# Kernel optimization log

Measured on AMD Instinct MI355X. Metric: run time of the kernel, lower is better.

## Reference

```python
import jax, jax.numpy as jnp
import numpy as np

D_MODEL = 1024
D_STATE = 16
D_CONV = 4
EXPAND = 2
D_INNER = EXPAND * D_MODEL  # 2048
DT_RANK = 64  # ceil(1024/16)
BATCH = 2
SEQ = 1024
EPS = 1e-5


def _causal_depthwise_conv(x, w, b):
    # x: (B, L, D); w: (D, K) depthwise kernel; b: (D,)
    K = w.shape[1]
    xp = jnp.pad(x, ((0, 0), (K - 1, 0), (0, 0)))            # left-pad for causality
    out = jax.lax.conv_general_dilated(
        xp.transpose(0, 2, 1),          # (B, D, L+K-1)
        w[:, None, :],                  # (D, 1, K)
        window_strides=(1,), padding='VALID',
        feature_group_count=w.shape[0])
    return out.transpose(0, 2, 1) + b   # (B, L, D)


def _ssm_dir(xs, conv_w, conv_b, xproj_w, dt_w, dt_b, A_log, D_skip):
    # xs: (B, L, D_INNER)
    Bsz = xs.shape[0]
    xc = jax.nn.silu(_causal_depthwise_conv(xs, conv_w, conv_b))
    x_dbl = xc @ xproj_w                                        # (B, L, dt_rank + 2N)
    dt, B_ssm, C_ssm = jnp.split(x_dbl, [DT_RANK, DT_RANK + D_STATE], axis=-1)
    dt = jax.nn.softplus(dt @ dt_w + dt_b)                      # (B, L, D_INNER)
    A = -jnp.exp(A_log)                                         # (D_INNER, N)
    dA = jnp.exp(dt[..., None] * A)                             # (B, L, D_INNER, N)
    dBu = dt[..., None] * B_ssm[:, :, None, :] * xc[..., None]  # (B, L, D_INNER, N)

    def step(h, inp):
        dAt, dBut, ct = inp          # (B,D,N), (B,D,N), (B,N)
        h = dAt * h + dBut
        y = jnp.einsum('bdn,bn->bd', h, ct)
        return h, y

    h0 = jnp.zeros((Bsz, D_INNER, D_STATE), dtype=xs.dtype)
    _, ys = jax.lax.scan(step, h0,
                         (jnp.moveaxis(dA, 1, 0), jnp.moveaxis(dBu, 1, 0), jnp.moveaxis(C_ssm, 1, 0)))
    y = jnp.moveaxis(ys, 0, 1)                                  # (B, L, D_INNER)
    return y + xc * D_skip


def _layernorm(x, gamma, beta):
    mu = jnp.mean(x, axis=-1, keepdims=True)
    var = jnp.mean(jnp.square(x - mu), axis=-1, keepdims=True)
    return (x - mu) * jax.lax.rsqrt(var + EPS) * gamma + beta


def setup_inputs() -> dict:
    key = jax.random.key(0)
    ks = jax.random.split(key, 24)
    s = 0.02
    A_init = jnp.log(jnp.tile(jnp.arange(1, D_STATE + 1, dtype=jnp.float32)[None, :], (D_INNER, 1)))
    # dt bias init (inverse-softplus of small dt), as in the torch module
    dt0 = jnp.exp(jax.random.uniform(ks[20], (D_INNER,)) * (np.log(0.1) - np.log(0.001)) + np.log(0.001))
    dt0 = jnp.clip(dt0, 1e-4)
    inv_dt = dt0 + jnp.log(-jnp.expm1(-dt0))
    return {
        'x': jax.random.normal(ks[0], (BATCH, SEQ, D_MODEL), jnp.float32),
        'gamma': jnp.ones((D_MODEL,), jnp.float32),
        'beta': jnp.zeros((D_MODEL,), jnp.float32),
        'in_w': jax.random.normal(ks[1], (D_MODEL, 2 * D_INNER), jnp.float32) * s,
        'conv_w': jax.random.normal(ks[2], (D_INNER, D_CONV), jnp.float32) * s,
        'conv_b': jnp.zeros((D_INNER,), jnp.float32),
        'xproj_w': jax.random.normal(ks[3], (D_INNER, DT_RANK + 2 * D_STATE), jnp.float32) * s,
        'dt_w': jax.random.normal(ks[4], (DT_RANK, D_INNER), jnp.float32) * s,
        'dt_b': inv_dt,
        'A_log': A_init,
        'D_skip': jnp.ones((D_INNER,), jnp.float32),
        'conv_w_b': jax.random.normal(ks[5], (D_INNER, D_CONV), jnp.float32) * s,
        'conv_b_b': jnp.zeros((D_INNER,), jnp.float32),
        'xproj_w_b': jax.random.normal(ks[6], (D_INNER, DT_RANK + 2 * D_STATE), jnp.float32) * s,
        'dt_w_b': jax.random.normal(ks[7], (DT_RANK, D_INNER), jnp.float32) * s,
        'dt_b_b': inv_dt,
        'A_log_b': A_init,
        'D_skip_b': jnp.ones((D_INNER,), jnp.float32),
        'merge_w': jax.random.normal(ks[8], (2 * D_INNER, D_INNER), jnp.float32) * s,
        'out_w': jax.random.normal(ks[9], (D_INNER, D_MODEL), jnp.float32) * s,
    }


def reference(x, gamma, beta, in_w, conv_w, conv_b, xproj_w, dt_w, dt_b, A_log, D_skip,
              conv_w_b, conv_b_b, xproj_w_b, dt_w_b, dt_b_b, A_log_b, D_skip_b,
              merge_w, out_w):
    residual = x
    h = _layernorm(x, gamma, beta)
    xz = h @ in_w                               # (B, L, 2*D_INNER)
    xs, z = jnp.split(xz, 2, axis=-1)
    y_fwd = _ssm_dir(xs, conv_w, conv_b, xproj_w, dt_w, dt_b, A_log, D_skip)
    y_back = _ssm_dir(xs[:, ::-1], conv_w_b, conv_b_b, xproj_w_b, dt_w_b, dt_b_b, A_log_b, D_skip_b)[:, ::-1]
    y = jnp.concatenate([y_fwd, y_back], axis=-1) @ merge_w
    y = y * jax.nn.silu(z)
    y = y @ out_w
    return residual + y
```

## Files before the change

### kernel.cpp

```cpp
#include <hip/hip_runtime.h>
#include <hip/hip_bf16.h>
#include <math.h>

typedef __hip_bfloat16 bf16;
typedef unsigned int u32;
typedef __attribute__((ext_vector_type(8))) short bf16x8;
typedef __attribute__((ext_vector_type(4))) float f32x4;

#define BATCH 2
#define SEQ 1024
#define DM 1024
#define DI 2048
#define NST 16
#define DTR 64
#define XDN 96
#define XDP_LD 128
#define T_TOK 2048
#define N2 4096
#define NCHUNK 32
#define CLEN 32

static __device__ __forceinline__ float b2f(bf16 v) { return __bfloat162float(v); }
static __device__ __forceinline__ float bits2f(unsigned short u) {
    return __uint_as_float(((unsigned)u) << 16);
}

static __device__ __forceinline__ float softplus_fast(float t) {
    return (t > 20.f) ? t : __logf(1.f + __expf(t));
}

static __device__ __forceinline__ void gload_lds16(const void* g, void* l) {
    __builtin_amdgcn_global_load_lds((__attribute__((address_space(1))) u32*)(size_t)g,
                                     (__attribute__((address_space(3))) u32*)l, 16, 0, 0);
}

#define SBAR() do { asm volatile("" ::: "memory"); __builtin_amdgcn_s_barrier(); asm volatile("" ::: "memory"); } while (0)

static __device__ void tileT(const float* __restrict__ in, bf16* __restrict__ out,
                             int K, int N, int t, float (*tb)[33]) {
    int nt = N >> 5;
    int bx = (t % nt) << 5, by = (t / nt) << 5;
    int tx = threadIdx.x & 31, r0 = threadIdx.x >> 5;
#pragma unroll
    for (int r = r0; r < 32; r += 8)
        tb[r][tx] = in[(size_t)(by + r) * N + bx + tx];
    __syncthreads();
#pragma unroll
    for (int r = r0; r < 32; r += 8)
        out[(size_t)(bx + r) * K + by + tx] = __float2bfloat16(tb[tx][r]);
}

#define LN_BLKS   T_TOK
#define INW_T     ((N2 / 32) * (DM / 32))
#define OUTW_T    ((DM / 32) * (DI / 32))
#define MRGW_T    ((DI / 32) * (N2 / 32))
#define SMALL_BLK ((2 * XDP_LD * DI + 2 * DI * DTR) / 256)

__global__ __launch_bounds__(256) void prep_mega(const float* __restrict__ x,
                                                 const float* __restrict__ gamma,
                                                 const float* __restrict__ beta,
                                                 bf16* __restrict__ H,
                                                 const float* __restrict__ in_w, bf16* __restrict__ in_wT,
                                                 const float* __restrict__ out_w, bf16* __restrict__ out_wT,
                                                 const float* __restrict__ merge_w, bf16* __restrict__ merge_wT,
                                                 const float* __restrict__ xpf, const float* __restrict__ xpb,
                                                 bf16* __restrict__ XPF, bf16* __restrict__ XPB,
                                                 const float* __restrict__ dtwf, const float* __restrict__ dtwb,
                                                 bf16* __restrict__ dtwT) {
    __shared__ float tbuf[32][33];
    __shared__ float red[8];
    int bid = blockIdx.x;
    int tid = threadIdx.x;

    if (bid < LN_BLKS) {
        int t = bid;
        float xv[4];
        float s = 0.f, s2 = 0.f;
#pragma unroll
        for (int k = 0; k < 4; ++k) {
            float v = x[(size_t)t * DM + k * 256 + tid];
            xv[k] = v; s += v; s2 += v * v;
        }
#pragma unroll
        for (int off = 32; off; off >>= 1) {
            s  += __shfl_down(s, off);
            s2 += __shfl_down(s2, off);
        }
        int wid = tid >> 6, lane = tid & 63;
        if (!lane) { red[wid] = s; red[4 + wid] = s2; }
        __syncthreads();
        if (tid == 0) {
            float S = red[0] + red[1] + red[2] + red[3];
            float S2 = red[4] + red[5] + red[6] + red[7];
            float mu = S * (1.f / DM);
            float var = S2 * (1.f / DM) - mu * mu;
            red[0] = mu;
            red[1] = rsqrtf(var + 1e-5f);
        }
        __syncthreads();
        float mu = red[0], rs = red[1];
#pragma unroll
        for (int k = 0; k < 4; ++k) {
            int i = k * 256 + tid;
            H[(size_t)t * DM + i] = __float2bfloat16((xv[k] - mu) * rs * gamma[i] + beta[i]);
        }
        return;
    }
    bid -= LN_BLKS;
    if (bid < INW_T)  { tileT(in_w, in_wT, DM, N2, bid, tbuf); return; }
    bid -= INW_T;
    if (bid < OUTW_T) { tileT(out_w, out_wT, DI, DM, bid, tbuf); return; }
    bid -= OUTW_T;
    if (bid < MRGW_T) { tileT(merge_w, merge_wT, N2, DI, bid, tbuf); return; }
    bid -= MRGW_T;
    int idx = bid * 256 + tid;
    if (idx < 2 * XDP_LD * DI) {
        int dir = idx >= XDP_LD * DI;
        int i = idx - dir * (XDP_LD * DI);
        int n = i >> 11;
        int k = i & (DI - 1);
        float v = (n < XDN) ? (dir ? xpb : xpf)[k * XDN + n] : 0.f;
        (dir ? XPB : XPF)[i] = __float2bfloat16(v);
    } else {
        int j = idx - 2 * XDP_LD * DI;
        int dir = j >= DI * DTR;
        int e = j - dir * (DI * DTR);
        int n = e >> 6;
        int k = e & 63;
        dtwT[(size_t)dir * DI * DTR + n * DTR + k] =
            __float2bfloat16((dir ? dtwb : dtwf)[(size_t)k * DI + n]);
    }
}

template <int EPI>
__global__ __launch_bounds__(256) void mfma_gemm(const bf16* __restrict__ A,
                                                 const bf16* __restrict__ BT,
                                                 const bf16* __restrict__ BT2, int bysplit,
                                                 bf16* __restrict__ Cb,
                                                 const float* __restrict__ resid,
                                                 float* __restrict__ outf,
                                                 bf16* __restrict__ Pb,
                                                 const float* __restrict__ bias1,
                                                 const float* __restrict__ bias2,
                                                 int M, int N, int K) {
    __shared__ bf16 As[8192];
    __shared__ bf16 Bs[8192];
    int tid = threadIdx.x;
    int wave = tid >> 6, lane = tid & 63;
    int q = lane >> 4, ln16 = lane & 15;
    int bm = blockIdx.y * 128, bn = blockIdx.x * 128;
    int wm = (wave >> 1) * 64, wn = (wave & 1) * 64;
    const bf16* Bt = ((int)blockIdx.y < bysplit) ? BT : BT2;

    int ks = K / gridDim.z;
    int kb = blockIdx.z * ks;

    f32x4 zf; zf[0] = zf[1] = zf[2] = zf[3] = 0.f;
    f32x4 acc[4][4];
#pragma unroll
    for (int i = 0; i < 4; ++i)
#pragma unroll
        for (int j = 0; j < 4; ++j) acc[i][j] = zf;

    for (int k0 = kb; k0 < kb + ks; k0 += 64) {
#pragma unroll
        for (int i = 0; i < 4; ++i) {
            int s = wave * 256 + i * 64 + lane;
            int kg = s >> 7, m = s & 127;
            gload_lds16(&A[(size_t)(bm + m) * K + k0 + kg * 8], &As[(wave * 256 + i * 64) * 8]);
            gload_lds16(&Bt[(size_t)(bn + m) * K + k0 + kg * 8], &Bs[(wave * 256 + i * 64) * 8]);
        }
        __syncthreads();
#pragma unroll
        for (int kk = 0; kk < 2; ++kk) {
            bf16x8 af[4], bfr[4];
#pragma unroll
            for (int i = 0; i < 4; ++i) {
                af[i]  = *(const bf16x8*)&As[(((kk * 4 + q) * 128) + (wm + i * 16 + ln16)) * 8];
                bfr[i] = *(const bf16x8*)&Bs[(((kk * 4 + q) * 128) + (wn + i * 16 + ln16)) * 8];
            }
#pragma unroll
            for (int i = 0; i < 4; ++i)
#pragma unroll
                for (int j = 0; j < 4; ++j)
                    acc[i][j] = __builtin_amdgcn_mfma_f32_16x16x32_bf16(af[i], bfr[j], acc[i][j], 0, 0, 0);
        }
        __syncthreads();
    }

    size_t pbase = (size_t)blockIdx.z * M * N;
#pragma unroll
    for (int i = 0; i < 4; ++i)
#pragma unroll
        for (int r = 0; r < 4; ++r) {
            int row = bm + wm + i * 16 + q * 4 + r;
            const float* bias = (EPI == 4) ? ((row < T_TOK) ? bias1 : bias2) : nullptr;
#pragma unroll
            for (int j = 0; j < 4; ++j) {
                int col = bn + wn + j * 16 + ln16;
                size_t idx = (size_t)row * N + col;
                float v = acc[i][j][r];
                if (EPI == 0)      Cb[idx] = __float2bfloat16(v);
                else if (EPI == 1) outf[idx] = resid[idx] + v;
                else if (EPI == 2) outf[idx] = v;
                else if (EPI == 3) Pb[pbase + idx] = __float2bfloat16(v);
                else {
                    Cb[idx] = __float2bfloat16(softplus_fast(v + bias[col]));
                }
            }
        }
}

template <int EPI>
__global__ __launch_bounds__(512, 2) void gemm256(const bf16* __restrict__ A,
                                                  const bf16* __restrict__ BT,
                                                  bf16* __restrict__ Cb,
                                                  bf16* __restrict__ Pb,
                                                  int M, int N, int K) {
    __shared__ bf16 LA[4][8192];
    __shared__ bf16 LB[4][8192];
    int tid = threadIdx.x;
    int wave = tid >> 6, lane = tid & 63;
    int q = lane >> 4, ln16 = lane & 15;

    int gx = gridDim.x, gy = gridDim.y, gz = gridDim.z;
    int L = blockIdx.x + gx * (blockIdx.y + gy * blockIdx.z);
    int nwg = gx * gy * gz;
    int qd = nwg >> 3, rd = nwg & 7;
    int xcd = L & 7, base = L >> 3;
    int wg = (xcd < rd ? xcd * (qd + 1) : rd * (qd + 1) + (xcd - rd) * qd) + base;
    int bxi = wg % gx, byi = (wg / gx) % gy, bzi = wg / (gx * gy);

    int bm = byi * 256, bn = bxi * 256;
    int wm = (wave >> 2) * 128, wn = (wave & 3) * 64;
    int ksz = K / gz;
    int kb = bzi * ksz;
    int NT = ksz >> 5;

    int o0 = tid * 16, o1 = 8192 + tid * 16;
    int r0 = o0 >> 6, r1 = o1 >> 6;
    int c0 = (o0 & 63) ^ (((r0 >> 1) & 3) << 4);
    int c1 = (o1 & 63) ^ (((r1 >> 1) & 3) << 4);
    const bf16* pa0 = &A[(size_t)(bm + r0) * K + kb + (c0 >> 1)];
    const bf16* pa1 = &A[(size_t)(bm + r1) * K + kb + (c1 >> 1)];
    const bf16* pb0 = &BT[(size_t)(bn + r0) * K + kb + (c0 >> 1)];
    const bf16* pb1 = &BT[(size_t)(bn + r1) * K + kb + (c1 >> 1)];
    int d0 = wave * 512;
    int d1 = 4096 + wave * 512;

    int aoff[8], boff[4];
#pragma unroll
    for (int i = 0; i < 8; ++i) {
        int r = wm + i * 16 + ln16;
        aoff[i] = (r * 64 + q * 16) ^ (((r >> 1) & 3) << 4);
    }
#pragma unroll
    for (int j = 0; j < 4; ++j) {
        int r = wn + j * 16 + ln16;
        boff[j] = (r * 64 + q * 16) ^ (((r >> 1) & 3) << 4);
    }

    f32x4 zf; zf[0] = zf[1] = zf[2] = zf[3] = 0.f;
    f32x4 acc[8][4];
#pragma unroll
    for (int i = 0; i < 8; ++i)
#pragma unroll
        for (int j = 0; j < 4; ++j) acc[i][j] = zf;

    auto STAGE = [&](int b, int koff) {
        gload_lds16(pa0 + koff, &LA[b][d0]);
        gload_lds16(pa1 + koff, &LA[b][d1]);
        gload_lds16(pb0 + koff, &LB[b][d0]);
        gload_lds16(pb1 + koff, &LB[b][d1]);
    };

#define RD_FRAGS(AV, BV, TT) do {                                             \
        const bf16* LAb_ = LA[(TT) & 3];                                      \
        const bf16* LBb_ = LB[(TT) & 3];                                      \
        _Pragma("unroll")                                                     \
        for (int j_ = 0; j_ < 4; ++j_) BV[j_] = *(const bf16x8*)&LBb_[boff[j_] >> 1]; \
        _Pragma("unroll")                                                     \
        for (int i_ = 0; i_ < 8; ++i_) AV[i_] = *(const bf16x8*)&LAb_[aoff[i_] >> 1]; \
    } while (0)

#define MFMA_ALL(AV, BV) do {                                                 \
        __builtin_amdgcn_s_setprio(1);                                        \
        _Pragma("unroll")                                                     \
        for (int i_ = 0; i_ < 8; ++i_)                                        \
            _Pragma("unroll")                                                 \
            for (int j_ = 0; j_ < 4; ++j_)                                    \
                acc[i_][j_] = __builtin_amdgcn_mfma_f32_16x16x32_bf16(AV[i_], BV[j_], acc[i_][j_], 0, 0, 0); \
        __builtin_amdgcn_s_setprio(0);                                        \
    } while (0)

    bf16x8 avX[8], bvX[4], avY[8], bvY[4];

    STAGE(0, 0); STAGE(1, 32); STAGE(2, 64);
    asm volatile("s_waitcnt vmcnt(4)" ::: "memory");
    SBAR();
    RD_FRAGS(avX, bvX, 0);

    for (int t = 0; t < NT; t += 2) {
        if (t + 1 < NT) RD_FRAGS(avY, bvY, t + 1);
        if (t + 3 < NT) STAGE((t + 3) & 3, (t + 3) * 32);
        MFMA_ALL(avX, bvX);
        if (t + 3 < NT)      asm volatile("s_waitcnt vmcnt(4)" ::: "memory");
        else if (t + 2 < NT) asm volatile("s_waitcnt vmcnt(0)" ::: "memory");
        SBAR();
        if (t + 2 < NT) RD_FRAGS(avX, bvX, t + 2);
        if (t + 4 < NT) STAGE((t + 4) & 3, (t + 4) * 32);
        MFMA_ALL(avY, bvY);
        if (t + 4 < NT)      asm volatile("s_waitcnt vmcnt(4)" ::: "memory");
        else if (t + 3 < NT) asm volatile("s_waitcnt vmcnt(0)" ::: "memory");
        SBAR();
    }
#undef RD_FRAGS
#undef MFMA_ALL

    size_t pbase = (size_t)bzi * ((size_t)M * N);
#pragma unroll
    for (int i = 0; i < 8; ++i)
#pragma unroll
        for (int r = 0; r < 4; ++r) {
            int row = bm + wm + i * 16 + q * 4 + r;
#pragma unroll
            for (int j = 0; j < 4; ++j) {
                int col = bn + wn + j * 16 + ln16;
                size_t idx = (size_t)row * N + col;
                float v = acc[i][j][r];
                if (EPI == 0) Cb[idx] = __float2bfloat16(v);
                else          Pb[pbase + idx] = __float2bfloat16(v);
            }
        }
}

__global__ __launch_bounds__(256) void reduce_plain(const bf16* __restrict__ P, int ns, size_t MN,
                                                    bf16* __restrict__ O) {
    size_t i = ((size_t)blockIdx.x * 256 + threadIdx.x) * 4;
    float s[4] = {0.f, 0.f, 0.f, 0.f};
    for (int k = 0; k < ns; ++k) {
        ushort4 p = *reinterpret_cast<const ushort4*>(&P[(size_t)k * MN + i]);
        s[0] += bits2f(p.x); s[1] += bits2f(p.y); s[2] += bits2f(p.z); s[3] += bits2f(p.w);
    }
    bf16 r[4];
#pragma unroll
    for (int j = 0; j < 4; ++j) r[j] = __float2bfloat16(s[j]);
    *reinterpret_cast<ushort4*>(&O[i]) = *reinterpret_cast<ushort4*>(r);
}

__global__ __launch_bounds__(256) void reduce_gate(const bf16* __restrict__ P, int ns, size_t MN,
                                                   const bf16* __restrict__ XZ, bf16* __restrict__ YM) {
    size_t i = ((size_t)blockIdx.x * 256 + threadIdx.x) * 4;
    float s[4] = {0.f, 0.f, 0.f, 0.f};
    for (int k = 0; k < ns; ++k) {
        ushort4 p = *reinterpret_cast<const ushort4*>(&P[(size_t)k * MN + i]);
        s[0] += bits2f(p.x); s[1] += bits2f(p.y); s[2] += bits2f(p.z); s[3] += bits2f(p.w);
    }
    int t = (int)(i >> 11), c = (int)(i & (DI - 1));
    const bf16* zp = &XZ[(size_t)t * N2 + DI + c];
    bf16 r[4];
#pragma unroll
    for (int j = 0; j < 4; ++j) {
        float z = b2f(zp[j]);
        r[j] = __float2bfloat16(s[j] * (z / (1.f + __expf(-z))));
    }
    *reinterpret_cast<ushort4*>(&YM[i]) = *reinterpret_cast<ushort4*>(r);
}

__global__ __launch_bounds__(256) void reduce_out(const bf16* __restrict__ P, int ns, size_t MN,
                                                  const float* __restrict__ x, float* __restrict__ out) {
    size_t i = ((size_t)blockIdx.x * 256 + threadIdx.x) * 4;
    float s[4] = {0.f, 0.f, 0.f, 0.f};
    for (int k = 0; k < ns; ++k) {
        ushort4 p = *reinterpret_cast<const ushort4*>(&P[(size_t)k * MN + i]);
        s[0] += bits2f(p.x); s[1] += bits2f(p.y); s[2] += bits2f(p.z); s[3] += bits2f(p.w);
    }
    float4 xv = *reinterpret_cast<const float4*>(&x[i]);
    float4 o = {s[0] + xv.x, s[1] + xv.y, s[2] + xv.z, s[3] + xv.w};
    *reinterpret_cast<float4*>(&out[i]) = o;
}

__global__ __launch_bounds__(256) void reduce_xdbl(const bf16* __restrict__ P, int ns, size_t MN,
                                                   float* __restrict__ XDP, bf16* __restrict__ XDdt) {
    size_t i = ((size_t)blockIdx.x * 256 + threadIdx.x) * 4;
    float s[4] = {0.f, 0.f, 0.f, 0.f};
    for (int k = 0; k < ns; ++k) {
        ushort4 p = *reinterpret_cast<const ushort4*>(&P[(size_t)k * MN + i]);
        s[0] += bits2f(p.x); s[1] += bits2f(p.y); s[2] += bits2f(p.z); s[3] += bits2f(p.w);
    }
    float4 o = {s[0], s[1], s[2], s[3]};
    *reinterpret_cast<float4*>(&XDP[i]) = o;
    int col = (int)(i & (XDP_LD - 1));
    if (col < DTR) {
        size_t row = i >> 7;
        bf16 r[4];
#pragma unroll
        for (int j = 0; j < 4; ++j) r[j] = __float2bfloat16(s[j]);
        *reinterpret_cast<ushort4*>(&XDdt[row * DTR + col]) = *reinterpret_cast<ushort4*>(r);
    }
}

__global__ __launch_bounds__(256) void gemm_dt(const float* __restrict__ A,
                                               const float* __restrict__ Bw,
                                               const float* __restrict__ bias,
                                               bf16* __restrict__ Cb, int M, int N) {
    __shared__ float As[16][68];
    __shared__ float Bs[16][68];
    int tid = threadIdx.x;
    int bm = blockIdx.y * 64, bn = blockIdx.x * 64;
    int tx = tid & 15, ty = tid >> 4;
    float acc[4][4];
#pragma unroll
    for (int i = 0; i < 4; ++i)
#pragma unroll
        for (int j = 0; j < 4; ++j) acc[i][j] = 0.f;
    int arow = tid >> 2, acg = (tid & 3) * 4;
    int brow = tid >> 4, bcol = (tid & 15) * 4;
    for (int k0 = 0; k0 < DTR; k0 += 16) {
        float4 av = *reinterpret_cast<const float4*>(&A[(size_t)(bm + arow) * XDP_LD + k0 + acg]);
        As[acg + 0][arow] = av.x; As[acg + 1][arow] = av.y;
        As[acg + 2][arow] = av.z; As[acg + 3][arow] = av.w;
        float4 bv = *reinterpret_cast<const float4*>(&Bw[(size_t)(k0 + brow) * N + bn + bcol]);
        Bs[brow][bcol + 0] = bv.x; Bs[brow][bcol + 1] = bv.y;
        Bs[brow][bcol + 2] = bv.z; Bs[brow][bcol + 3] = bv.w;
        __syncthreads();
#pragma unroll
        for (int kk = 0; kk < 16; ++kk) {
            float4 a = *reinterpret_cast<const float4*>(&As[kk][ty * 4]);
            float4 b = *reinterpret_cast<const float4*>(&Bs[kk][tx * 4]);
            acc[0][0] += a.x * b.x; acc[0][1] += a.x * b.y; acc[0][2] += a.x * b.z; acc[0][3] += a.x * b.w;
            acc[1][0] += a.y * b.x; acc[1][1] += a.y * b.y; acc[1][2] += a.y * b.z; acc[1][3] += a.y * b.w;
            acc[2][0] += a.z * b.x; acc[2][1] += a.z * b.y; acc[2][2] += a.z * b.z; acc[2][3] += a.z * b.w;
            acc[3][0] += a.w * b.x; acc[3][1] += a.w * b.y; acc[3][2] += a.w * b.z; acc[3][3] += a.w * b.w;
        }
        __syncthreads();
    }
    int row0 = bm + ty * 4, col0 = bn + tx * 4;
#pragma unroll
    for (int i = 0; i < 4; ++i)
#pragma unroll
        for (int j = 0; j < 4; ++j) {
            float v = acc[i][j] + bias[col0 + j];
            Cb[(size_t)(row0 + i) * N + col0 + j] = __float2bfloat16(softplus_fast(v));
        }
}

__global__ __launch_bounds__(256) void conv_kernel(const bf16* __restrict__ XZ,
                                                   const float* __restrict__ wf, const float* __restrict__ bf_,
                                                   const float* __restrict__ wb, const float* __restrict__ bb_,
                                                   bf16* __restrict__ XCF, bf16* __restrict__ XCB) {
    int idx = blockIdx.x * 256 + threadIdx.x;
    int cg = idx & (DI / 8 - 1);
    int c0 = cg * 8;
    int g = idx >> 8;
    int l = g & (SEQ - 1);
    int b = g >> 10;
    float sf[8], sb[8];
    float4 wfv[8], wbv[8];
#pragma unroll
    for (int u = 0; u < 8; ++u) {
        wfv[u] = *(const float4*)&wf[(c0 + u) * 4];
        wbv[u] = *(const float4*)&wb[(c0 + u) * 4];
        sf[u] = bf_[c0 + u];
        sb[u] = bb_[c0 + u];
    }
#pragma unroll
    for (int j = 0; j < 4; ++j) {
        int lf = l - 3 + j;
        if (lf >= 0) {
            bf16x8 v = *(const bf16x8*)&XZ[((size_t)(b * SEQ + lf)) * N2 + c0];
#pragma unroll
            for (int u = 0; u < 8; ++u) {
                float w = (j == 0) ? wfv[u].x : (j == 1) ? wfv[u].y : (j == 2) ? wfv[u].z : wfv[u].w;
                sf[u] += w * bits2f((unsigned short)v[u]);
            }
        }
        int lb = l + 3 - j;
        if (lb < SEQ) {
            bf16x8 v = *(const bf16x8*)&XZ[((size_t)(b * SEQ + lb)) * N2 + c0];
#pragma unroll
            for (int u = 0; u < 8; ++u) {
                float w = (j == 0) ? wbv[u].x : (j == 1) ? wbv[u].y : (j == 2) ? wbv[u].z : wbv[u].w;
                sb[u] += w * bits2f((unsigned short)v[u]);
            }
        }
    }
    bf16 rf[8], rb[8];
#pragma unroll
    for (int u = 0; u < 8; ++u) {
        rf[u] = __float2bfloat16(sf[u] / (1.f + __expf(-sf[u])));
        rb[u] = __float2bfloat16(sb[u] / (1.f + __expf(-sb[u])));
    }
    size_t o = (size_t)g * DI + c0;
    *(bf16x8*)&XCF[o] = *(bf16x8*)rf;
    *(bf16x8*)&XCB[o] = *(bf16x8*)rb;
}

template <int NC, bool FINAL>
__global__ __launch_bounds__(256) void scan_chunk(const bf16* __restrict__ DTF_, const bf16* __restrict__ DTB_,
                                                  const bf16* __restrict__ XCF_, const bf16* __restrict__ XCB_,
                                                  const float* __restrict__ XDP,
                                                  const float* __restrict__ Af, const float* __restrict__ Ab,
                                                  const float* __restrict__ Df, const float* __restrict__ Db,
                                                  float* __restrict__ HLOC, float* __restrict__ SUMDT,
                                                  bf16* __restrict__ YCAT) {
    constexpr int CL = SEQ / NC;
    __shared__ float bsl[CL][32];
    __shared__ bf16 dtl[CL][128];
    __shared__ bf16 xcl[CL][128];
    int tid = threadIdx.x;
    int sg = tid & 1;
    int cl = tid >> 1;
    int cbase = blockIdx.x * 128;
    int c = cbase + cl;
    int b = blockIdx.y;
    int dir = (int)blockIdx.z >= NC;
    int chunk = blockIdx.z - dir * NC;
    const bf16* DT = dir ? DTB_ : DTF_;
    const bf16* XC = dir ? XCB_ : XCF_;
    for (int i = tid; i < CL * 8; i += 256) {
        int it = i >> 3, j4 = (i & 7) * 4;
        int sit = chunk * CL + it;
        int l = dir ? (SEQ - 1 - sit) : sit;
        size_t row = (size_t)dir * T_TOK + (size_t)b * SEQ + l;
        *(float4*)&bsl[it][j4] = *(const float4*)&XDP[row * XDP_LD + DTR + j4];
    }
    for (int ch = tid; ch < CL * 16; ch += 256) {
        int it = ch >> 4, of = (ch & 15) * 8;
        int sit = chunk * CL + it;
        int l = dir ? (SEQ - 1 - sit) : sit;
        size_t g = (size_t)b * SEQ + l;
        *(bf16x8*)&dtl[it][of] = *(const bf16x8*)&DT[g * DI + cbase + of];
        *(bf16x8*)&xcl[it][of] = *(const bf16x8*)&XC[g * DI + cbase + of];
    }
    const float* Al = dir ? Ab : Af;
    int sg8 = sg * 8;
    float A[8];
#pragma unroll
    for (int n = 0; n < 8; ++n) A[n] = -__expf(Al[c * NST + sg8 + n]);
    float aunit = A[0] / (float)(sg8 + 1);
    bool fastp = true;
#pragma unroll
    for (int n = 1; n < 8; ++n) {
        float k = A[n] / aunit;
        fastp = fastp && (fabsf(k - (float)(sg8 + 1 + n)) < 1e-3f);
    }
    size_t base = ((((size_t)dir * BATCH + b) * NC + chunk) * DI + c);
    float h[8];
    float Dv = 0.f;
    if (FINAL) {
#pragma unroll
        for (int n = 0; n < 8; ++n) h[n] = HLOC[base * NST + sg8 + n];
        Dv = (dir ? Db : Df)[c];
    } else {
#pragma unroll
        for (int n = 0; n < 8; ++n) h[n] = 0.f;
    }
    __syncthreads();
    float sumdt = 0.f;
    for (int it = 0; it < CL; ++it) {
        int sit = chunk * CL + it;
        int l = dir ? (SEQ - 1 - sit) : sit;
        size_t g = (size_t)b * SEQ + l;
        float dt = b2f(dtl[it][cl]);
        float xc = b2f(xcl[it][cl]);
        float dtxc = dt * xc;
        const float* bs = &bsl[it][sg8];
        float da[8];
        if (fastp) {
            float r = __expf(dt * aunit);
            float p = r;
            if (sg) { float r2 = r * r; float r4 = r2 * r2; float r8 = r4 * r4; p = r8 * r; }
            da[0] = p;
#pragma unroll
            for (int n = 1; n < 8; ++n) { p *= r; da[n] = p; }
        } else {
#pragma unroll
            for (int n = 0; n < 8; ++n) da[n] = __expf(dt * A[n]);
        }
        if (FINAL) {
            float y = 0.f;
#pragma unroll
            for (int n = 0; n < 8; ++n) {
                h[n] = da[n] * h[n] + dtxc * bs[n];
                y += h[n] * bs[NST + n];
            }
            y += __shfl_xor(y, 1);
            if (!sg) YCAT[g * N2 + dir * DI + c] = __float2bfloat16(y + xc * Dv);
        } else {
            sumdt += dt;
#pragma unroll
            for (int n = 0; n < 8; ++n)
                h[n] = da[n] * h[n] + dtxc * bs[n];
        }
    }
    if (!FINAL) {
#pragma unroll
        for (int n = 0; n < 8; ++n) HLOC[base * NST + sg8 + n] = h[n];
        if (!sg) SUMDT[base] = sumdt;
    }
}

__global__ __launch_bounds__(256) void scan_combine(float* __restrict__ HLOC,
                                                    const float* __restrict__ SUMDT,
                                                    const float* __restrict__ Af,
                                                    const float* __restrict__ Ab, int nchunk) {
    int idx = blockIdx.x * 256 + threadIdx.x;
    int n = idx & 15;
    int c = (idx >> 4) & (DI - 1);
    int b = (idx >> 15) & 1;
    int dir = idx >> 16;
    float A = -__expf((dir ? Ab : Af)[c * NST + n]);
    float h = 0.f;
    for (int k = 0; k < nchunk; ++k) {
        size_t base = ((((size_t)dir * BATCH + b) * nchunk + k) * DI + c);
        float P = __expf(A * SUMDT[base]);
        float hl = HLOC[base * NST + n];
        HLOC[base * NST + n] = h;
        h = P * h + hl;
    }
}

__global__ __launch_bounds__(256) void gate_kernel(bf16* __restrict__ YM, const bf16* __restrict__ XZ) {
    int idx = blockIdx.x * 256 + threadIdx.x;
    int t = idx >> 11;
    int c = idx & (DI - 1);
    float z = b2f(XZ[(size_t)t * N2 + DI + c]);
    float y = b2f(YM[idx]);
    YM[idx] = __float2bfloat16(y * (z / (1.f + __expf(-z))));
}

extern "C" void kernel_launch(void* const* d_in, const int* in_sizes, int n_in,
                              void* d_out, int out_size, void* d_ws, size_t ws_size,
                              hipStream_t stream) {
    const float* x       = (const float*)d_in[0];
    const float* gamma   = (const float*)d_in[1];
    const float* beta    = (const float*)d_in[2];
    const float* in_w    = (const float*)d_in[3];
    const float* conv_w  = (const float*)d_in[4];
    const float* conv_b  = (const float*)d_in[5];
    const float* xproj_w = (const float*)d_in[6];
    const float* dt_w    = (const float*)d_in[7];
    const float* dt_b    = (const float*)d_in[8];
    const float* A_log   = (const float*)d_in[9];
    const float* D_skip  = (const float*)d_in[10];
    const float* conv_w_b  = (const float*)d_in[11];
    const float* conv_b_b  = (const float*)d_in[12];
    const float* xproj_w_b = (const float*)d_in[13];
    const float* dt_w_b    = (const float*)d_in[14];
    const float* dt_b_b    = (const float*)d_in[15];
    const float* A_log_b   = (const float*)d_in[16];
    const float* D_skip_b  = (const float*)d_in[17];
    const float* merge_w   = (const float*)d_in[18];
    const float* out_w     = (const float*)d_in[19];
    float* out = (float*)d_out;

    char* w = (char*)d_ws;
    size_t off = 0;
    bf16* H       = (bf16*)(w + off); off += (size_t)T_TOK * DM * 2;
    bf16* XZ      = (bf16*)(w + off); off += (size_t)T_TOK * N2 * 2;
    bf16* XCF     = (bf16*)(w + off); off += (size_t)T_TOK * DI * 2;
    bf16* XCB     = (bf16*)(w + off); off += (size_t)T_TOK * DI * 2;
    bf16* XPF     = (bf16*)(w + off); off += (size_t)XDP_LD * DI * 2;
    bf16* XPB     = (bf16*)(w + off); off += (size_t)XDP_LD * DI * 2;
    float* XDP    = (float*)(w + off); off += (size_t)2 * T_TOK * XDP_LD * 4;
    bf16* DTF     = (bf16*)(w + off); off += (size_t)T_TOK * DI * 2;
    bf16* DTB     = (bf16*)(w + off); off += (size_t)T_TOK * DI * 2;
    bf16* YCAT    = (bf16*)(w + off); off += (size_t)T_TOK * N2 * 2;
    bf16* in_wT   = (bf16*)(w + off); off += (size_t)N2 * DM * 2;
    bf16* out_wT  = (bf16*)(w + off); off += (size_t)DM * DI * 2;
    bf16* merge_wT= (bf16*)(w + off); off += (size_t)DI * N2 * 2;
    bf16* dtwT    = (bf16*)(w + off); off += (size_t)2 * DI * DTR * 2;
    bf16* XDdt    = (bf16*)(w + off); off += (size_t)2 * T_TOK * DTR * 2;
    char* PART = w + off;
    size_t avail = (ws_size > off) ? ws_size - off : 0;

    float* HLOC  = (float*)PART;
    float* SUMDT = (float*)(PART + (size_t)2 * BATCH * NCHUNK * DI * NST * 4);
    bf16* Pb     = (bf16*)PART;
    bf16* YM     = DTF;

    size_t MNm = (size_t)T_TOK * DI;
    size_t MNo = (size_t)T_TOK * DM;
    size_t MNx = (size_t)2 * T_TOK * XDP_LD;
    size_t MNz = (size_t)T_TOK * N2;
    int s_merge = (avail >= 4 * MNm * 2) ? 4 : (avail >= 2 * MNm * 2) ? 2 : 0;
    int s_out   = (avail >= 4 * MNo * 2) ? 4 : (avail >= 2 * MNo * 2) ? 2 : 0;
    int s_xdbl  = (avail >= 16 * MNx * 2) ? 16 : (avail >= 8 * MNx * 2) ? 8 : (avail >= 4 * MNx * 2) ? 4 : 0;
    int s_xz    = (avail >= 2 * MNz * 2) ? 2 : 0;

    prep_mega<<<LN_BLKS + INW_T + OUTW_T + MRGW_T + SMALL_BLK, 256, 0, stream>>>(
        x, gamma, beta, H, in_w, in_wT, out_w, out_wT, merge_w, merge_wT,
        xproj_w, xproj_w_b, XPF, XPB, dt_w, dt_w_b, dtwT);
    if (s_xz) {
        gemm256<3><<<dim3(N2 / 256, T_TOK / 256, s_xz), 512, 0, stream>>>(
            H, in_wT, nullptr, Pb, T_TOK, N2, DM);
        reduce_plain<<<(int)(MNz / 4 / 256), 256, 0, stream>>>(Pb, s_xz, MNz, XZ);
    } else {
        mfma_gemm<0><<<dim3(N2 / 128, T_TOK / 128), 256, 0, stream>>>(
            H, in_wT, in_wT, 1 << 30, XZ, nullptr, nullptr, nullptr, nullptr, nullptr, T_TOK, N2, DM);
    }
    conv_kernel<<<(T_TOK * DI / 8) / 256, 256, 0, stream>>>(XZ, conv_w, conv_b, conv_w_b, conv_b_b, XCF, XCB);
    if (s_xdbl) {
        mfma_gemm<3><<<dim3(1, (2 * T_TOK) / 128, s_xdbl), 256, 0, stream>>>(
            XCF, XPF, XPB, (T_TOK / 128), nullptr, nullptr, nullptr, Pb, nullptr, nullptr,
            2 * T_TOK, XDP_LD, DI);
        reduce_xdbl<<<(int)(MNx / 4 / 256), 256, 0, stream>>>(Pb, s_xdbl, MNx, XDP, XDdt);
        mfma_gemm<4><<<dim3(DI / 128, (2 * T_TOK) / 128), 256, 0, stream>>>(
            XDdt, dtwT, dtwT + (size_t)DI * DTR, (T_TOK / 128), DTF, nullptr, nullptr, nullptr,
            dt_b, dt_b_b, 2 * T_TOK, DI, DTR);
    } else {
        mfma_gemm<2><<<dim3(1, (2 * T_TOK) / 128), 256, 0, stream>>>(
            XCF, XPF, XPB, (T_TOK / 128), nullptr, nullptr, XDP, nullptr, nullptr, nullptr,
            2 * T_TOK, XDP_LD, DI);
        gemm_dt<<<dim3(DI / 64, T_TOK / 64), 256, 0, stream>>>(XDP, dt_w, dt_b, DTF, T_TOK, DI);
        gemm_dt<<<dim3(DI / 64, T_TOK / 64), 256, 0, stream>>>(XDP + (size_t)T_TOK * XDP_LD, dt_w_b, dt_b_b, DTB, T_TOK, DI);
    }
    scan_chunk<NCHUNK, false><<<dim3(DI / 128, BATCH, 2 * NCHUNK), 256, 0, stream>>>(
        DTF, DTB, XCF, XCB, XDP, A_log, A_log_b, D_skip, D_skip_b, HLOC, SUMDT, YCAT);
    scan_combine<<<(2 * BATCH * DI * NST) / 256, 256, 0, stream>>>(HLOC, SUMDT, A_log, A_log_b, NCHUNK);
    scan_chunk<NCHUNK, true><<<dim3(DI / 128, BATCH, 2 * NCHUNK), 256, 0, stream>>>(
        DTF, DTB, XCF, XCB, XDP, A_log, A_log_b, D_skip, D_skip_b, HLOC, SUMDT, YCAT);
    if (s_merge) {
        gemm256<3><<<dim3(DI / 256, T_TOK / 256, s_merge), 512, 0, stream>>>(
            YCAT, merge_wT, nullptr, Pb, T_TOK, DI, N2);
        reduce_gate<<<(int)(MNm / 4 / 256), 256, 0, stream>>>(Pb, s_merge, MNm, XZ, YM);
    } else {
        mfma_gemm<0><<<dim3(DI / 128, T_TOK / 128), 256, 0, stream>>>(
            YCAT, merge_wT, merge_wT, 1 << 30, YM, nullptr, nullptr, nullptr, nullptr, nullptr,
            T_TOK, DI, N2);
        gate_kernel<<<(T_TOK * DI) / 256, 256, 0, stream>>>(YM, XZ);
    }
    if (s_out) {
        mfma_gemm<3><<<dim3(DM / 128, T_TOK / 128, s_out), 256, 0, stream>>>(
            YM, out_wT, out_wT, 1 << 30, nullptr, nullptr, nullptr, Pb, nullptr, nullptr,
            T_TOK, DM, DI);
        reduce_out<<<(int)(MNo / 4 / 256), 256, 0, stream>>>(Pb, s_out, MNo, x, out);
    } else {
        mfma_gemm<1><<<dim3(DM / 128, T_TOK / 128), 256, 0, stream>>>(
            YM, out_wT, out_wT, 1 << 30, nullptr, x, out, nullptr, nullptr, nullptr,
            T_TOK, DM, DI);
    }
}
```

Before: 388.0 us.

## Shrink gemm256 tile to 256x128 with triple-buffered LDS and higher occupancy

The big split-K GEMM kernel moves from a 256x256 block tile with 4-stage LDS buffering and 8x4 accumulator fragments per wave to a 256x128 tile with 3-stage buffering and 4x4 fragments per wave. The launch bound rises to 4 blocks per CU, and the grid doubles in the N dimension. The aim is less LDS and register pressure, more resident workgroups and more blocks to fill the GPU. In exchange, each block reuses data less, its software pipeline is simpler with no double-buffered fragments, and global traffic per FLOP goes up.

```diff
diff --git a/kernel.cpp b/kernel.cpp
--- a/kernel.cpp
+++ b/kernel.cpp
@@ -212,13 +212,13 @@
 }
 
 template <int EPI>
-__global__ __launch_bounds__(512, 2) void gemm256(const bf16* __restrict__ A,
+__global__ __launch_bounds__(512, 4) void gemm256(const bf16* __restrict__ A,
                                                   const bf16* __restrict__ BT,
                                                   bf16* __restrict__ Cb,
                                                   bf16* __restrict__ Pb,
                                                   int M, int N, int K) {
-    __shared__ bf16 LA[4][8192];
-    __shared__ bf16 LB[4][8192];
+    __shared__ bf16 LA[3][8192];
+    __shared__ bf16 LB[3][4096];
     int tid = threadIdx.x;
     int wave = tid >> 6, lane = tid & 63;
     int q = lane >> 4, ln16 = lane & 15;
@@ -231,95 +231,75 @@
     int wg = (xcd < rd ? xcd * (qd + 1) : rd * (qd + 1) + (xcd - rd) * qd) + base;
     int bxi = wg % gx, byi = (wg / gx) % gy, bzi = wg / (gx * gy);
 
-    int bm = byi * 256, bn = bxi * 256;
-    int wm = (wave >> 2) * 128, wn = (wave & 3) * 64;
+    int bm = byi * 256, bn = bxi * 128;
+    int wm = (wave >> 1) * 64, wn = (wave & 1) * 64;
     int ksz = K / gz;
     int kb = bzi * ksz;
     int NT = ksz >> 5;
 
-    int o0 = tid * 16, o1 = 8192 + tid * 16;
-    int r0 = o0 >> 6, r1 = o1 >> 6;
-    int c0 = (o0 & 63) ^ (((r0 >> 1) & 3) << 4);
-    int c1 = (o1 & 63) ^ (((r1 >> 1) & 3) << 4);
-    const bf16* pa0 = &A[(size_t)(bm + r0) * K + kb + (c0 >> 1)];
-    const bf16* pa1 = &A[(size_t)(bm + r1) * K + kb + (c1 >> 1)];
-    const bf16* pb0 = &BT[(size_t)(bn + r0) * K + kb + (c0 >> 1)];
-    const bf16* pb1 = &BT[(size_t)(bn + r1) * K + kb + (c1 >> 1)];
-    int d0 = wave * 512;
-    int d1 = 4096 + wave * 512;
-
-    int aoff[8], boff[4];
-#pragma unroll
-    for (int i = 0; i < 8; ++i) {
+    int rl = tid >> 2;
+    int cB = ((tid & 3) * 16) ^ (((rl >> 1) & 3) << 4);
+    const bf16* pa0 = &A[(size_t)(bm + rl) * K + kb + (cB >> 1)];
+    const bf16* pa1 = pa0 + (size_t)128 * K;
+    const bf16* pb  = &BT[(size_t)(bn + rl) * K + kb + (cB >> 1)];
+    int dA0 = wave * 512, dA1 = 4096 + wave * 512, dB = wave * 512;
+
+    int aoff[4], boff[4];
+#pragma unroll
+    for (int i = 0; i < 4; ++i) {
         int r = wm + i * 16 + ln16;
-        aoff[i] = (r * 64 + q * 16) ^ (((r >> 1) & 3) << 4);
+        aoff[i] = r * 64 + ((q * 16) ^ (((r >> 1) & 3) << 4));
     }
 #pragma unroll
     for (int j = 0; j < 4; ++j) {
         int r = wn + j * 16 + ln16;
-        boff[j] = (r * 64 + q * 16) ^ (((r >> 1) & 3) << 4);
+        boff[j] = r * 64 + ((q * 16) ^ (((r >> 1) & 3) << 4));
     }
 
     f32x4 zf; zf[0] = zf[1] = zf[2] = zf[3] = 0.f;
-    f32x4 acc[8][4];
-#pragma unroll
-    for (int i = 0; i < 8; ++i)
+    f32x4 acc[4][4];
+#pragma unroll
+    for (int i = 0; i < 4; ++i)
 #pragma unroll
         for (int j = 0; j < 4; ++j) acc[i][j] = zf;
 
-    auto STAGE = [&](int b, int koff) {
-        gload_lds16(pa0 + koff, &LA[b][d0]);
-        gload_lds16(pa1 + koff, &LA[b][d1]);
-        gload_lds16(pb0 + koff, &LB[b][d0]);
-        gload_lds16(pb1 + koff, &LB[b][d1]);
+    auto STAGE = [&](int b, int t) {
+        gload_lds16(pa0 + t * 32, &LA[b][dA0]);
+        gload_lds16(pa1 + t * 32, &LA[b][dA1]);
+        gload_lds16(pb  + t * 32, &LB[b][dB]);
     };
 
-#define RD_FRAGS(AV, BV, TT) do {                                             \
-        const bf16* LAb_ = LA[(TT) & 3];                                      \
-        const bf16* LBb_ = LB[(TT) & 3];                                      \
-        _Pragma("unroll")                                                     \
-        for (int j_ = 0; j_ < 4; ++j_) BV[j_] = *(const bf16x8*)&LBb_[boff[j_] >> 1]; \
-        _Pragma("unroll")                                                     \
-        for (int i_ = 0; i_ < 8; ++i_) AV[i_] = *(const bf16x8*)&LAb_[aoff[i_] >> 1]; \
-    } while (0)
-
-#define MFMA_ALL(AV, BV) do {                                                 \
-        __builtin_amdgcn_s_setprio(1);                                        \
-        _Pragma("unroll")                                                     \
-        for (int i_ = 0; i_ < 8; ++i_)                                        \
-            _Pragma("unroll")                                                 \
-            for (int j_ = 0; j_ < 4; ++j_)                                    \
-                acc[i_][j_] = __builtin_amdgcn_mfma_f32_16x16x32_bf16(AV[i_], BV[j_], acc[i_][j_], 0, 0, 0); \
-        __builtin_amdgcn_s_setprio(0);                                        \
-    } while (0)
-
-    bf16x8 avX[8], bvX[4], avY[8], bvY[4];
-
-    STAGE(0, 0); STAGE(1, 32); STAGE(2, 64);
-    asm volatile("s_waitcnt vmcnt(4)" ::: "memory");
+    STAGE(0, 0); STAGE(1, 1);
+    asm volatile("s_waitcnt vmcnt(3)" ::: "memory");
     SBAR();
-    RD_FRAGS(avX, bvX, 0);
-
-    for (int t = 0; t < NT; t += 2) {
-        if (t + 1 < NT) RD_FRAGS(avY, bvY, t + 1);
-        if (t + 3 < NT) STAGE((t + 3) & 3, (t + 3) * 32);
-        MFMA_ALL(avX, bvX);
-        if (t + 3 < NT)      asm volatile("s_waitcnt vmcnt(4)" ::: "memory");
-        else if (t + 2 < NT) asm volatile("s_waitcnt vmcnt(0)" ::: "memory");
+
+    int bc = 0, bs = 2;
+    for (int t = 0; t < NT; ++t) {
+        const bf16* Ab = LA[bc];
+        const bf16* Bb = LB[bc];
+        bf16x8 af[4], bfr[4];
+#pragma unroll
+        for (int j = 0; j < 4; ++j) bfr[j] = *(const bf16x8*)&Bb[boff[j] >> 1];
+#pragma unroll
+        for (int i = 0; i < 4; ++i) af[i] = *(const bf16x8*)&Ab[aoff[i] >> 1];
+        if (t + 2 < NT) STAGE(bs, t + 2);
+        __builtin_amdgcn_s_setprio(1);
+#pragma unroll
+        for (int i = 0; i < 4; ++i)
+#pragma unroll
+            for (int j = 0; j < 4; ++j)
+                acc[i][j] = __builtin_amdgcn_mfma_f32_16x16x32_bf16(af[i], bfr[j], acc[i][j], 0, 0, 0);
+        __builtin_amdgcn_s_setprio(0);
+        if (t + 2 < NT)      asm volatile("s_waitcnt vmcnt(3)" ::: "memory");
+        else if (t + 1 < NT) asm volatile("s_waitcnt vmcnt(0)" ::: "memory");
         SBAR();
-        if (t + 2 < NT) RD_FRAGS(avX, bvX, t + 2);
-        if (t + 4 < NT) STAGE((t + 4) & 3, (t + 4) * 32);
-        MFMA_ALL(avY, bvY);
-        if (t + 4 < NT)      asm volatile("s_waitcnt vmcnt(4)" ::: "memory");
-        else if (t + 3 < NT) asm volatile("s_waitcnt vmcnt(0)" ::: "memory");
-        SBAR();
-    }
-#undef RD_FRAGS
-#undef MFMA_ALL
+        bc = (bc == 2) ? 0 : bc + 1;
+        bs = (bs == 2) ? 0 : bs + 1;
+    }
 
     size_t pbase = (size_t)bzi * ((size_t)M * N);
 #pragma unroll
-    for (int i = 0; i < 8; ++i)
+    for (int i = 0; i < 4; ++i)
 #pragma unroll
         for (int r = 0; r < 4; ++r) {
             int row = bm + wm + i * 16 + q * 4 + r;
@@ -693,7 +673,7 @@
         x, gamma, beta, H, in_w, in_wT, out_w, out_wT, merge_w, merge_wT,
         xproj_w, xproj_w_b, XPF, XPB, dt_w, dt_w_b, dtwT);
     if (s_xz) {
-        gemm256<3><<<dim3(N2 / 256, T_TOK / 256, s_xz), 512, 0, stream>>>(
+        gemm256<3><<<dim3(N2 / 128, T_TOK / 256, s_xz), 512, 0, stream>>>(
             H, in_wT, nullptr, Pb, T_TOK, N2, DM);
         reduce_plain<<<(int)(MNz / 4 / 256), 256, 0, stream>>>(Pb, s_xz, MNz, XZ);
     } else {
@@ -722,7 +702,7 @@
     scan_chunk<NCHUNK, true><<<dim3(DI / 128, BATCH, 2 * NCHUNK), 256, 0, stream>>>(
         DTF, DTB, XCF, XCB, XDP, A_log, A_log_b, D_skip, D_skip_b, HLOC, SUMDT, YCAT);
     if (s_merge) {
-        gemm256<3><<<dim3(DI / 256, T_TOK / 256, s_merge), 512, 0, stream>>>(
+        gemm256<3><<<dim3(DI / 128, T_TOK / 256, s_merge), 512, 0, stream>>>(
             YCAT, merge_wT, nullptr, Pb, T_TOK, DI, N2);
         reduce_gate<<<(int)(MNm / 4 / 256), 256, 0, stream>>>(Pb, s_merge, MNm, XZ, YM);
     } else {
```

After: 387.5 us. No clear change (-0.1%).
